# Optimization experiments

Hardware: AMD Instinct MI355X
Metric: run time of the kernel (lower is better)

## Reference

```python
import jax, jax.numpy as jnp
import numpy as np

N_QUBIT = 20
N_LAYER = 50
FEAT = 128
BATCH = 128
N_NODES = BATCH * N_QUBIT * (N_LAYER + 1)  # 130560
N_EDGES = 524288
VOCAB = N_QUBIT * (N_LAYER + 1) + 1  # 1021
NEG_SLOPE = 0.01


def setup_inputs() -> dict:
    key = jax.random.key(0)
    ks = jax.random.split(key, 32)
    s = 0.05
    x = jax.random.randint(ks[0], (N_NODES,), 0, VOCAB, dtype=jnp.int64 if jax.config.read('jax_enable_x64') else jnp.int32)
    edge_index = jax.random.randint(ks[1], (2, N_EDGES), 0, N_NODES, dtype=x.dtype)
    emb = (jax.random.normal(ks[2], (VOCAB, FEAT), jnp.float32) * s).at[0].set(0.0)  # padding_idx=0
    gcn_w = jax.random.normal(ks[3], (5, FEAT, FEAT), jnp.float32) * s
    gcn_b = jnp.zeros((5, FEAT), jnp.float32)
    mlp_dims = [(2 * FEAT, 2 * FEAT), (2 * FEAT, FEAT), (FEAT, FEAT), (FEAT, FEAT // 2), (FEAT // 2, FEAT // 2), (FEAT // 2, 1)]
    mlp = {}
    for i, (din, dout) in enumerate(mlp_dims):
        mlp[f'mw{i}'] = jax.random.normal(ks[4 + i], (din, dout), jnp.float32) * s
        mlp[f'mb{i}'] = jnp.zeros((dout,), jnp.float32)
    return dict(x=x, edge_index=edge_index, emb=emb, gcn_w=gcn_w, gcn_b=gcn_b, **mlp)


def _leaky(v):
    return jnp.where(v >= 0, v, NEG_SLOPE * v)


def _gcn(h, src, dst, W, b):
    # PyG GCNConv: h' = D^-1/2 (A+I) D^-1/2 (h W) + b, flow src -> dst
    n = h.shape[0]
    hw = h @ W
    loops = jnp.arange(n, dtype=src.dtype)
    s2 = jnp.concatenate([src, loops])
    d2 = jnp.concatenate([dst, loops])
    deg = jax.ops.segment_sum(jnp.ones(s2.shape[0], hw.dtype), d2, num_segments=n)
    dinv = jnp.where(deg > 0, jax.lax.rsqrt(deg), 0.0)
    norm = dinv[s2] * dinv[d2]  # [E+N]
    out = jax.ops.segment_sum(hw[s2] * norm[:, None], d2, num_segments=n)
    return out + b


def reference(x, edge_index, emb, gcn_w, gcn_b, mw0, mb0, mw1, mb1, mw2, mb2, mw3, mb3, mw4, mb4, mw5, mb5):
    src, dst = edge_index[0], edge_index[1]
    h = emb[x]  # [N, f]
    for i in range(4):
        h = _leaky(_gcn(h, src, dst, gcn_w[i], gcn_b[i])) + h
    h = _gcn(h, src, dst, gcn_w[4], gcn_b[4]) + h
    n, f = N_QUBIT, FEAT
    h = h.reshape(-1, n * (N_LAYER + 1), f)[:, :n, :]  # [B, n, f]
    b = h.shape[0]
    # cartesian pairs (i, j): concat(h_i, h_j) -> [B, n, n, 2f]
    xi = jnp.broadcast_to(h[:, :, None, :], (b, n, n, f))
    xj = jnp.broadcast_to(h[:, None, :, :], (b, n, n, f))
    p = jnp.concatenate([xi, xj], axis=-1)
    p = _leaky(p @ mw0 + mb0)
    p = _leaky(p @ mw1 + mb1)
    p = _leaky(p @ mw2 + mb2)
    p = _leaky(p @ mw3 + mb3)
    p = _leaky(p @ mw4 + mb4)
    p = (p @ mw5 + mb5)[..., 0]  # [B, n, n]
    p = (p + jnp.swapaxes(p, -1, -2)) / 2
    return p.reshape(-1, n * n)
```

## Files before the change

### kernel.cpp

```cpp
#include <hip/hip_runtime.h>
#include <hip/hip_bf16.h>

#define NQ 20
#define NLAY 51
#define FEAT 128
#define BATCH 128
#define NN (BATCH * NQ * NLAY)
#define NE 524288
#define NPAIR (BATCH * NQ * NQ)
#define NB (NN / 256)
#define VOCAB 1021

typedef _Float16 half8 __attribute__((ext_vector_type(8)));
typedef float floatx4 __attribute__((ext_vector_type(4)));
typedef unsigned int uint;

__device__ __forceinline__ float lrelu(float v) { return v >= 0.f ? v : 0.01f * v; }

__device__ __forceinline__ uint packhl(float v) {
    _Float16 h = (_Float16)v;
    _Float16 l = (_Float16)(v - (float)h);
    union { _Float16 f; unsigned short u; } hb, lb;
    hb.f = h; lb.f = l;
    return (uint)hb.u | ((uint)lb.u << 16);
}

__device__ __forceinline__ void unpack8(uint4 a, uint4 b, half8& hi, half8& lo) {
    union { uint u[4]; half8 h; } H, L;
    H.u[0] = __builtin_amdgcn_perm(a.y, a.x, 0x05040100u);
    H.u[1] = __builtin_amdgcn_perm(a.w, a.z, 0x05040100u);
    H.u[2] = __builtin_amdgcn_perm(b.y, b.x, 0x05040100u);
    H.u[3] = __builtin_amdgcn_perm(b.w, b.z, 0x05040100u);
    L.u[0] = __builtin_amdgcn_perm(a.y, a.x, 0x07060302u);
    L.u[1] = __builtin_amdgcn_perm(a.w, a.z, 0x07060302u);
    L.u[2] = __builtin_amdgcn_perm(b.y, b.x, 0x07060302u);
    L.u[3] = __builtin_amdgcn_perm(b.w, b.z, 0x07060302u);
    hi = H.h;
    lo = L.h;
}

__global__ void k_count(const int* __restrict__ dst, int* __restrict__ cnt) {
    int e = blockIdx.x * 256 + threadIdx.x;
    atomicAdd(&cnt[dst[e]], 1);
}

__global__ void k_offsets(const int* __restrict__ cnt, const int* __restrict__ x,
                          int* __restrict__ offs, float* __restrict__ dinv,
                          int4* __restrict__ meta, int* __restrict__ cursor,
                          int* __restrict__ flag1, int* __restrict__ idmap) {
    __shared__ int sm[256];
    __shared__ int sbase;
    int t = threadIdx.x, g = blockIdx.x * 256 + t;
    int v = cnt[g];
    sm[t] = v;
    __syncthreads();
    for (int s = 1; s < 256; s <<= 1) {
        int add = (t >= s) ? sm[t - s] : 0;
        __syncthreads();
        sm[t] += add;
        __syncthreads();
    }
    if (t == 255) sbase = atomicAdd(cursor, sm[255]);
    __syncthreads();
    int off = sbase + sm[t] - v;
    float di = rsqrtf((float)(v + 1));
    offs[g] = off;
    dinv[g] = di;
    meta[g] = make_int4(off, v, __float_as_int(di), x[g]);
    if (g % (NQ * NLAY) < NQ) flag1[g] = 1;
    if (g < 1024) idmap[g] = min(g, VOCAB - 1);
}

__global__ void k_fill(const int* __restrict__ src, const int* __restrict__ dst,
                       const int* __restrict__ offs, int* __restrict__ fill,
                       const float* __restrict__ dinv, const int* __restrict__ x,
                       int2* __restrict__ csre, int2* __restrict__ csre0,
                       int* __restrict__ flag1) {
    int e = blockIdx.x * 256 + threadIdx.x;
    int d = dst[e];
    int s = src[e];
    int pos = offs[d] + atomicAdd(&fill[d], 1);
    int wb = __float_as_int(dinv[s] * dinv[d]);
    csre[pos] = make_int2(s, wb);
    csre0[pos] = make_int2(x[s], wb);
    if (d % (NQ * NLAY) < NQ) flag1[s] = 1;
}

__global__ void k_s1pass(const int* __restrict__ flagI, const int4* __restrict__ meta,
                         const int2* __restrict__ csre, int* __restrict__ cur,
                         int4* __restrict__ recO, int* __restrict__ flagO,
                         int4* __restrict__ rec0q) {
    if (rec0q && blockIdx.x >= NB) {
        int q = (blockIdx.x - NB) * 256 + threadIdx.x;
        if (q < BATCH * NQ) {
            int b = q / NQ, i = q - b * NQ;
            int node = b * (NQ * NLAY) + i;
            int4 m = meta[node];
            float di = __int_as_float(m.z);
            int dc = min(m.y, 6);
            int2 eb[6];
#pragma unroll
            for (int j = 0; j < 6; j++) eb[j] = (j < dc) ? csre[m.x + j] : make_int2(0, 0);
            int4* r = rec0q + (size_t)q * 4;
            r[0] = make_int4(node + 1, m.y, __float_as_int(di * di), m.x);
            r[1] = make_int4(eb[0].x, eb[0].y, eb[1].x, eb[1].y);
            r[2] = make_int4(eb[2].x, eb[2].y, eb[3].x, eb[3].y);
            r[3] = make_int4(eb[4].x, eb[4].y, eb[5].x, eb[5].y);
        }
        return;
    }
    __shared__ int sm[256];
    __shared__ int sbase;
    int t = threadIdx.x, g = blockIdx.x * 256 + t;
    int v = flagI[g];
    sm[t] = v;
    __syncthreads();
    for (int s = 1; s < 256; s <<= 1) {
        int add = (t >= s) ? sm[t - s] : 0;
        __syncthreads();
        sm[t] += add;
        __syncthreads();
    }
    if (t == 255) sbase = atomicAdd(cur, sm[255]);
    __syncthreads();
    if (v) {
        int slot = sbase + sm[t] - 1;
        int4 m = meta[g];
        float di = __int_as_float(m.z);
        int dc = min(m.y, 6);
        int2 eb[6];
#pragma unroll
        for (int j = 0; j < 6; j++) eb[j] = (j < dc) ? csre[m.x + j] : make_int2(0, 0);
        int4* r = recO + (size_t)slot * 4;
        r[0] = make_int4(g + 1, m.y, __float_as_int(di * di), m.x);
        r[1] = make_int4(eb[0].x, eb[0].y, eb[1].x, eb[1].y);
        r[2] = make_int4(eb[2].x, eb[2].y, eb[3].x, eb[3].y);
        r[3] = make_int4(eb[4].x, eb[4].y, eb[5].x, eb[5].y);
        if (flagO) {
            flagO[g] = 1;
            for (int e = 0; e < m.y; e++) flagO[csre[m.x + e].x] = 1;
        }
    }
}

#define OFF_GCN 0
#define OFF_P0  81920
#define OFF_M1  147456
#define OFF_M2  180224
#define OFF_M3  196608
#define OFF_M4  204800
#define TS_TOTAL 208896

__global__ void k_tsplit_all(const float* __restrict__ gw, const float* __restrict__ mw0,
                             const float* __restrict__ mw1, const float* __restrict__ mw2,
                             const float* __restrict__ mw3, const float* __restrict__ mw4,
                             _Float16* __restrict__ hi, _Float16* __restrict__ lo) {
    int idx = blockIdx.x * 256 + threadIdx.x;
    const float* src;
    int K, N, rel;
    bool p0 = false;
    if (idx < OFF_P0) {
        int L = (idx - OFF_GCN) >> 14; rel = (idx - OFF_GCN) & 16383;
        src = gw + L * 16384; K = 128; N = 128;
    } else if (idx < OFF_M1) {
        rel = idx - OFF_P0; src = mw0; K = 128; N = 512; p0 = true;
    } else if (idx < OFF_M2) {
        rel = idx - OFF_M1;  src = mw1; K = 256; N = 128;
    } else if (idx < OFF_M3) {
        rel = idx - OFF_M2;  src = mw2; K = 128; N = 128;
    } else if (idx < OFF_M4) {
        rel = idx - OFF_M3;  src = mw3; K = 128; N = 64;
    } else {
        rel = idx - OFF_M4;  src = mw4; K = 64;  N = 64;
    }
    int kblks = K >> 5;
    int j = rel & 7;
    int lane = (rel >> 3) & 63;
    int t2 = rel >> 9;
    int kblk = t2 % kblks;
    int ntile = t2 / kblks;
    int col = ntile * 16 + (lane & 15);
    int k = kblk * 32 + ((lane >> 4) << 3) + j;
    float f;
    if (p0) {
        f = (col < 256) ? src[k * 256 + col] : src[(k + 128) * 256 + (col - 256)];
    } else {
        f = src[k * N + col];
    }
    _Float16 h = (_Float16)f;
    hi[idx] = h;
    lo[idx] = (_Float16)(f - (float)h);
}

template <int NT_N, bool LEAKY, bool BIAS, bool P0SPLIT, bool FUSEA, bool GATHA, bool LISTM>
__launch_bounds__(256, 2)
__global__ void hgemm(const float* __restrict__ A,
                      const float* __restrict__ FA, const float* __restrict__ FB,
                      const _Float16* __restrict__ Bh, const _Float16* __restrict__ Bl,
                      const float* __restrict__ bias,
                      float* __restrict__ C, float* __restrict__ C2,
                      int N, int K, const int* __restrict__ gmap,
                      const int* __restrict__ listm) {
    if (LISTM) {
        if ((unsigned)listm[blockIdx.x * 128] >= (unsigned)NN) return;
    }
    const int KB = K >> 5;
    const int lane = threadIdx.x & 63;
    const int wid = threadIdx.x >> 6;
    const int lm = lane & 15, lq = lane >> 4;
    const int m0 = blockIdx.x * 128 + wid * 32;
    const int n0t = blockIdx.y * NT_N;

    const float* arow[2];
    const float* brow[2];
#pragma unroll
    for (int mt = 0; mt < 2; mt++) {
        int row = m0 + mt * 16 + lm;
        if (FUSEA) {
            int b = row / (NQ * NQ);
            int rr = row - b * (NQ * NQ);
            int i = rr / NQ;
            int j = rr - i * NQ;
            arow[mt] = FA + (size_t)(b * NQ + i) * 256;
            brow[mt] = FB + (size_t)(b * NQ + j) * 256;
        } else if (GATHA) {
            arow[mt] = A + (size_t)gmap[row] * K;
        } else if (LISTM) {
            int lr = listm[row];
            lr = ((unsigned)lr < (unsigned)NN) ? lr : 0;
            arow[mt] = A + (size_t)lr * K;
        } else {
            arow[mt] = A + (size_t)row * K;
        }
    }

    floatx4 acc[2][NT_N];
#pragma unroll
    for (int mt = 0; mt < 2; mt++)
#pragma unroll
        for (int nt = 0; nt < NT_N; nt++) acc[mt][nt] = (floatx4)0.f;

    for (int kb = 0; kb < KB; kb++) {
        const int k0 = kb * 32 + lq * 8;
        half8 ahi[2], alo[2];
#pragma unroll
        for (int mt = 0; mt < 2; mt++) {
            floatx4 av0, av1;
            if (FUSEA) {
                floatx4 fa0 = *(const floatx4*)(arow[mt] + k0);
                floatx4 fa1 = *(const floatx4*)(arow[mt] + k0 + 4);
                floatx4 fb0 = *(const floatx4*)(brow[mt] + k0);
                floatx4 fb1 = *(const floatx4*)(brow[mt] + k0 + 4);
#pragma unroll
                for (int q = 0; q < 4; q++) {
                    av0[q] = lrelu(fa0[q] + fb0[q]);
                    av1[q] = lrelu(fa1[q] + fb1[q]);
                }
            } else {
                av0 = *(const floatx4*)(arow[mt] + k0);
                av1 = *(const floatx4*)(arow[mt] + k0 + 4);
            }
#pragma unroll
            for (int q = 0; q < 4; q++) {
                _Float16 h0 = (_Float16)av0[q];
                ahi[mt][q] = h0;
                alo[mt][q] = (_Float16)(av0[q] - (float)h0);
                _Float16 h1 = (_Float16)av1[q];
                ahi[mt][4 + q] = h1;
                alo[mt][4 + q] = (_Float16)(av1[q] - (float)h1);
            }
        }
#pragma unroll
        for (int nt = 0; nt < NT_N; nt++) {
            size_t boff = (((size_t)(n0t + nt) * KB + kb) * 64 + lane) * 8;
            half8 bhi = *(const half8*)(Bh + boff);
            half8 blo = *(const half8*)(Bl + boff);
#pragma unroll
            for (int mt = 0; mt < 2; mt++) {
                acc[mt][nt] = __builtin_amdgcn_mfma_f32_16x16x32_f16(ahi[mt], bhi, acc[mt][nt], 0, 0, 0);
                acc[mt][nt] = __builtin_amdgcn_mfma_f32_16x16x32_f16(ahi[mt], blo, acc[mt][nt], 0, 0, 0);
                acc[mt][nt] = __builtin_amdgcn_mfma_f32_16x16x32_f16(alo[mt], bhi, acc[mt][nt], 0, 0, 0);
            }
        }
    }

    int strow[2][4];
    bool svalid[2][4];
#pragma unroll
    for (int mt = 0; mt < 2; mt++)
#pragma unroll
        for (int r = 0; r < 4; r++) {
            int mlog = m0 + mt * 16 + lq * 4 + r;
            if (LISTM) {
                int sr = listm[mlog];
                svalid[mt][r] = (unsigned)sr < (unsigned)NN;
                strow[mt][r] = svalid[mt][r] ? sr : 0;
            } else {
                svalid[mt][r] = true;
                strow[mt][r] = mlog;
            }
        }

#pragma unroll
    for (int nt = 0; nt < NT_N; nt++) {
        int col = (n0t + nt) * 16 + lm;
        float bv = (BIAS || P0SPLIT) ? bias[col < 256 ? col : 0] : 0.f;
#pragma unroll
        for (int mt = 0; mt < 2; mt++) {
#pragma unroll
            for (int r = 0; r < 4; r++) {
                if (!svalid[mt][r]) continue;
                int row = strow[mt][r];
                float val = acc[mt][nt][r];
                if (P0SPLIT) {
                    if (col < 256) C[(size_t)row * 256 + col] = val + bv;
                    else C2[(size_t)row * 256 + col - 256] = val;
                } else {
                    if (BIAS) val += bv;
                    if (LEAKY) val = lrelu(val);
                    C[(size_t)row * N + col] = val;
                }
            }
        }
    }
}

template <bool LEAKY, bool FINAL>
__launch_bounds__(256, 8)
__global__ void k_lagg(const float* __restrict__ in, float* __restrict__ outp,
                       const int4* __restrict__ rec, const int2* __restrict__ csre,
                       const int* __restrict__ cntp, int fixcnt,
                       const _Float16* __restrict__ Bh, const _Float16* __restrict__ Bl,
                       const float* __restrict__ bias,
                       const _Float16* __restrict__ BhP, const _Float16* __restrict__ BlP,
                       const float* __restrict__ mb0p,
                       float* __restrict__ Abuf, float* __restrict__ Bbuf) {
    int lcnt = cntp ? *cntp : fixcnt;
    int sbase = blockIdx.x * 16;
    if (sbase >= lcnt) return;
    __shared__ uint X[16][132];
    __shared__ float R[16][132];
    __shared__ int NID[16];
    int tid = threadIdx.x;
    int sl = tid & 31;
    int grp = tid >> 5;
    const float4* in4 = (const float4*)in;
    {
        int lrow0 = grp * 2;
        int p0i = sbase + lrow0, p1i = p0i + 1;
        bool val0 = p0i < lcnt, val1 = p1i < lcnt;
        const int4* r0p = rec + (size_t)(val0 ? p0i : 0) * 4;
        const int4* r1p = rec + (size_t)(val1 ? p1i : 0) * 4;
        int4 hd0 = r0p[0], ea0 = r0p[1], eb0 = r0p[2], ec0 = r0p[3];
        int4 hd1 = r1p[0], ea1 = r1p[1], eb1 = r1p[2], ec1 = r1p[3];
        int n0 = hd0.x - 1;
        int n1 = hd1.x - 1;
        if (sl == 0) {
            NID[lrow0] = n0;
            NID[lrow0 + 1] = n1;
        }
        float s20 = __int_as_float(hd0.z), s21 = __int_as_float(hd1.z);
        float4 v0  = in4[(size_t)n0 * 32 + sl];
        float4 v1  = in4[(size_t)n1 * 32 + sl];
        float4 u00 = in4[(size_t)ea0.x * 32 + sl];
        float4 u01 = in4[(size_t)ea0.z * 32 + sl];
        float4 u02 = in4[(size_t)eb0.x * 32 + sl];
        float4 u03 = in4[(size_t)eb0.z * 32 + sl];
        float4 u04 = in4[(size_t)ec0.x * 32 + sl];
        float4 u05 = in4[(size_t)ec0.z * 32 + sl];
        float4 u10 = in4[(size_t)ea1.x * 32 + sl];
        float4 u11 = in4[(size_t)ea1.z * 32 + sl];
        float4 u12 = in4[(size_t)eb1.x * 32 + sl];
        float4 u13 = in4[(size_t)eb1.z * 32 + sl];
        float4 u14 = in4[(size_t)ec1.x * 32 + sl];
        float4 u15 = in4[(size_t)ec1.z * 32 + sl];
        *(float4*)&R[lrow0][sl * 4] = v0;
        *(float4*)&R[lrow0 + 1][sl * 4] = v1;
        float w00 = __int_as_float(ea0.y), w01 = __int_as_float(ea0.w);
        float w02 = __int_as_float(eb0.y), w03 = __int_as_float(eb0.w);
        float w04 = __int_as_float(ec0.y), w05 = __int_as_float(ec0.w);
        float w10 = __int_as_float(ea1.y), w11 = __int_as_float(ea1.w);
        float w12 = __int_as_float(eb1.y), w13 = __int_as_float(eb1.w);
        float w14 = __int_as_float(ec1.y), w15 = __int_as_float(ec1.w);
        float a0x = v0.x * s20 + u00.x * w00 + u01.x * w01 + u02.x * w02 + u03.x * w03 + u04.x * w04 + u05.x * w05;
        float a0y = v0.y * s20 + u00.y * w00 + u01.y * w01 + u02.y * w02 + u03.y * w03 + u04.y * w04 + u05.y * w05;
        float a0z = v0.z * s20 + u00.z * w00 + u01.z * w01 + u02.z * w02 + u03.z * w03 + u04.z * w04 + u05.z * w05;
        float a0w = v0.w * s20 + u00.w * w00 + u01.w * w01 + u02.w * w02 + u03.w * w03 + u04.w * w04 + u05.w * w05;
        float a1x = v1.x * s21 + u10.x * w10 + u11.x * w11 + u12.x * w12 + u13.x * w13 + u14.x * w14 + u15.x * w15;
        float a1y = v1.y * s21 + u10.y * w10 + u11.y * w11 + u12.y * w12 + u13.y * w13 + u14.y * w14 + u15.y * w15;
        float a1z = v1.z * s21 + u10.z * w10 + u11.z * w11 + u12.z * w12 + u13.z * w13 + u14.z * w14 + u15.z * w15;
        float a1w = v1.w * s21 + u10.w * w10 + u11.w * w11 + u12.w * w12 + u13.w * w13 + u14.w * w14 + u15.w * w15;
        int deg0 = val0 ? hd0.y : 0, deg1 = val1 ? hd1.y : 0;
        int dm = max(deg0, deg1);
        if (dm > 6) {
            int off0 = hd0.w, off1 = hd1.w;
            int d0c = max(deg0 - 1, 0), d1c = max(deg1 - 1, 0);
            for (int e = 6; e < dm; e += 6) {
                int2 e00 = csre[off0 + min(e,     d0c)];
                int2 e01 = csre[off0 + min(e + 1, d0c)];
                int2 e02 = csre[off0 + min(e + 2, d0c)];
                int2 e03 = csre[off0 + min(e + 3, d0c)];
                int2 e04 = csre[off0 + min(e + 4, d0c)];
                int2 e05 = csre[off0 + min(e + 5, d0c)];
                int2 e10 = csre[off1 + min(e,     d1c)];
                int2 e11 = csre[off1 + min(e + 1, d1c)];
                int2 e12 = csre[off1 + min(e + 2, d1c)];
                int2 e13 = csre[off1 + min(e + 3, d1c)];
                int2 e14 = csre[off1 + min(e + 4, d1c)];
                int2 e15 = csre[off1 + min(e + 5, d1c)];
                float4 x00 = in4[(size_t)e00.x * 32 + sl];
                float4 x01 = in4[(size_t)e01.x * 32 + sl];
                float4 x02 = in4[(size_t)e02.x * 32 + sl];
                float4 x03 = in4[(size_t)e03.x * 32 + sl];
                float4 x04 = in4[(size_t)e04.x * 32 + sl];
                float4 x05 = in4[(size_t)e05.x * 32 + sl];
                float4 x10 = in4[(size_t)e10.x * 32 + sl];
                float4 x11 = in4[(size_t)e11.x * 32 + sl];
                float4 x12 = in4[(size_t)e12.x * 32 + sl];
                float4 x13 = in4[(size_t)e13.x * 32 + sl];
                float4 x14 = in4[(size_t)e14.x * 32 + sl];
                float4 x15 = in4[(size_t)e15.x * 32 + sl];
                float q00 = (e     < deg0) ? __int_as_float(e00.y) : 0.f;
                float q01 = (e + 1 < deg0) ? __int_as_float(e01.y) : 0.f;
                float q02 = (e + 2 < deg0) ? __int_as_float(e02.y) : 0.f;
                float q03 = (e + 3 < deg0) ? __int_as_float(e03.y) : 0.f;
                float q04 = (e + 4 < deg0) ? __int_as_float(e04.y) : 0.f;
                float q05 = (e + 5 < deg0) ? __int_as_float(e05.y) : 0.f;
                float q10 = (e     < deg1) ? __int_as_float(e10.y) : 0.f;
                float q11 = (e + 1 < deg1) ? __int_as_float(e11.y) : 0.f;
                float q12 = (e + 2 < deg1) ? __int_as_float(e12.y) : 0.f;
                float q13 = (e + 3 < deg1) ? __int_as_float(e13.y) : 0.f;
                float q14 = (e + 4 < deg1) ? __int_as_float(e14.y) : 0.f;
                float q15 = (e + 5 < deg1) ? __int_as_float(e15.y) : 0.f;
                a0x += x00.x * q00 + x01.x * q01 + x02.x * q02 + x03.x * q03 + x04.x * q04 + x05.x * q05;
                a0y += x00.y * q00 + x01.y * q01 + x02.y * q02 + x03.y * q03 + x04.y * q04 + x05.y * q05;
                a0z += x00.z * q00 + x01.z * q01 + x02.z * q02 + x03.z * q03 + x04.z * q04 + x05.z * q05;
                a0w += x00.w * q00 + x01.w * q01 + x02.w * q02 + x03.w * q03 + x04.w * q04 + x05.w * q05;
                a1x += x10.x * q10 + x11.x * q11 + x12.x * q12 + x13.x * q13 + x14.x * q14 + x15.x * q15;
                a1y += x10.y * q10 + x11.y * q11 + x12.y * q12 + x13.y * q13 + x14.y * q14 + x15.y * q15;
                a1z += x10.z * q10 + x11.z * q11 + x12.z * q12 + x13.z * q13 + x14.z * q14 + x15.z * q15;
                a1w += x10.w * q10 + x11.w * q11 + x12.w * q12 + x13.w * q13 + x14.w * q14 + x15.w * q15;
            }
        }
        *(uint4*)&X[lrow0][sl * 4] =
            make_uint4(packhl(a0x), packhl(a0y), packhl(a0z), packhl(a0w));
        *(uint4*)&X[lrow0 + 1][sl * 4] =
            make_uint4(packhl(a1x), packhl(a1y), packhl(a1z), packhl(a1w));
    }
    __syncthreads();
    const int lane = tid & 63;
    const int wid = tid >> 6;
    const int lm = lane & 15, lq = lane >> 4;
    floatx4 acc[2];
    acc[0] = (floatx4)0.f;
    acc[1] = (floatx4)0.f;
#pragma unroll
    for (int kb = 0; kb < 4; kb++) {
        const int k0 = kb * 32 + lq * 8;
        uint4 pa = *(const uint4*)&X[lm][k0];
        uint4 pb = *(const uint4*)&X[lm][k0 + 4];
        half8 ahi, alo;
        unpack8(pa, pb, ahi, alo);
#pragma unroll
        for (int ntl = 0; ntl < 2; ntl++) {
            int nt = wid * 2 + ntl;
            size_t boff = (((size_t)nt * 4 + kb) * 64 + lane) * 8;
            half8 bhi = *(const half8*)(Bh + boff);
            half8 blo = *(const half8*)(Bl + boff);
            acc[ntl] = __builtin_amdgcn_mfma_f32_16x16x32_f16(ahi, bhi, acc[ntl], 0, 0, 0);
            acc[ntl] = __builtin_amdgcn_mfma_f32_16x16x32_f16(ahi, blo, acc[ntl], 0, 0, 0);
            acc[ntl] = __builtin_amdgcn_mfma_f32_16x16x32_f16(alo, bhi, acc[ntl], 0, 0, 0);
        }
    }
    if (FINAL) __syncthreads();
    int nodes[4];
    bool sval[4];
#pragma unroll
    for (int r = 0; r < 4; r++) {
        int slot = sbase + lq * 4 + r;
        sval[r] = slot < lcnt;
        nodes[r] = NID[lq * 4 + r];
    }
#pragma unroll
    for (int ntl = 0; ntl < 2; ntl++) {
        int col = (wid * 2 + ntl) * 16 + lm;
        float bv = bias[col];
#pragma unroll
        for (int r = 0; r < 4; r++) {
            if (!sval[r]) continue;
            float val = acc[ntl][r] + bv;
            if (LEAKY) val = lrelu(val);
            val += R[lq * 4 + r][col];
            if (FINAL)
                X[lq * 4 + r][col] = packhl(val);
            else
                outp[(size_t)nodes[r] * FEAT + col] = val;
        }
    }
    if (FINAL) {
        __syncthreads();
#pragma unroll
        for (int c = 0; c < 2; c++) {
            floatx4 acc4[4];
#pragma unroll
            for (int nt = 0; nt < 4; nt++) acc4[nt] = (floatx4)0.f;
#pragma unroll
            for (int kb = 0; kb < 4; kb++) {
                const int k0 = kb * 32 + lq * 8;
                uint4 pa = *(const uint4*)&X[lm][k0];
                uint4 pb = *(const uint4*)&X[lm][k0 + 4];
                half8 ahi, alo;
                unpack8(pa, pb, ahi, alo);
#pragma unroll
                for (int nt = 0; nt < 4; nt++) {
                    int T = wid * 8 + c * 4 + nt;
                    size_t boff = (((size_t)T * 4 + kb) * 64 + lane) * 8;
                    half8 bhi = *(const half8*)(BhP + boff);
                    half8 blo = *(const half8*)(BlP + boff);
                    acc4[nt] = __builtin_amdgcn_mfma_f32_16x16x32_f16(ahi, bhi, acc4[nt], 0, 0, 0);
                    acc4[nt] = __builtin_amdgcn_mfma_f32_16x16x32_f16(ahi, blo, acc4[nt], 0, 0, 0);
                    acc4[nt] = __builtin_amdgcn_mfma_f32_16x16x32_f16(alo, bhi, acc4[nt], 0, 0, 0);
                }
            }
#pragma unroll
            for (int nt = 0; nt < 4; nt++) {
                int T = wid * 8 + c * 4 + nt;
                int col = T * 16 + lm;
#pragma unroll
                for (int r = 0; r < 4; r++) {
                    int q = sbase + lq * 4 + r;
                    float val = acc4[nt][r];
                    if (col < 256) Abuf[(size_t)q * 256 + col] = val + mb0p[col];
                    else Bbuf[(size_t)q * 256 + col - 256] = val;
                }
            }
        }
    }
}

template <int KB, int NT>
__device__ __forceinline__ void pair_stage(uint (*__restrict__ X)[132],
                                           const _Float16* __restrict__ Bh,
                                           const _Float16* __restrict__ Bl,
                                           const float* __restrict__ bias,
                                           int srow, int lane) {
    const int lm = lane & 15, lq = lane >> 4;
    floatx4 acc[NT];
#pragma unroll
    for (int nt = 0; nt < NT; nt++) acc[nt] = (floatx4)0.f;
#pragma unroll
    for (int kb = 0; kb < KB; kb++) {
        const int k0 = kb * 32 + lq * 8;
        uint4 pa = *(const uint4*)&X[srow + lm][k0];
        uint4 pb = *(const uint4*)&X[srow + lm][k0 + 4];
        half8 ahi, alo;
        unpack8(pa, pb, ahi, alo);
#pragma unroll
        for (int nt = 0; nt < NT; nt++) {
            size_t boff = (((size_t)nt * KB + kb) * 64 + lane) * 8;
            half8 bhi = *(const half8*)(Bh + boff);
            half8 blo = *(const half8*)(Bl + boff);
            acc[nt] = __builtin_amdgcn_mfma_f32_16x16x32_f16(ahi, bhi, acc[nt], 0, 0, 0);
            acc[nt] = __builtin_amdgcn_mfma_f32_16x16x32_f16(ahi, blo, acc[nt], 0, 0, 0);
            acc[nt] = __builtin_amdgcn_mfma_f32_16x16x32_f16(alo, bhi, acc[nt], 0, 0, 0);
        }
    }
#pragma unroll
    for (int nt = 0; nt < NT; nt++) {
        int col = nt * 16 + lm;
        float bv = bias[col];
#pragma unroll
        for (int r = 0; r < 4; r++) {
            X[srow + lq * 4 + r][col] = packhl(lrelu(acc[nt][r] + bv));
        }
    }
}

__launch_bounds__(256, 4)
__global__ void k_pair(const float* __restrict__ FA, const float* __restrict__ FB,
                       const _Float16* __restrict__ bth, const _Float16* __restrict__ btl,
                       const float* __restrict__ mb1, const float* __restrict__ mb2,
                       const float* __restrict__ mb3, const float* __restrict__ mb4,
                       const float* __restrict__ mw5, const float* __restrict__ mb5,
                       float* __restrict__ out) {
    __shared__ uint X[64][132];
    const int lane = threadIdx.x & 63;
    const int wid = threadIdx.x >> 6;
    const int lm = lane & 15, lq = lane >> 4;
    const int srow = wid * 16;
    const int rbase = blockIdx.x * 64;

    {
        const int grow = rbase + srow + lm;
        int b = grow / (NQ * NQ);
        int rr = grow - b * (NQ * NQ);
        int i = rr / NQ;
        int j = rr - i * NQ;
        const float* arow = FA + (size_t)(b * NQ + i) * 256;
        const float* brow = FB + (size_t)(b * NQ + j) * 256;
        const _Float16* Bh = bth + OFF_M1;
        const _Float16* Bl = btl + OFF_M1;
        floatx4 acc[8];
#pragma unroll
        for (int nt = 0; nt < 8; nt++) acc[nt] = (floatx4)0.f;
        const int KB = 8;
#pragma unroll
        for (int kb = 0; kb < KB; kb++) {
            const int k0 = kb * 32 + lq * 8;
            floatx4 fa0 = *(const floatx4*)(arow + k0);
            floatx4 fa1 = *(const floatx4*)(arow + k0 + 4);
            floatx4 fb0 = *(const floatx4*)(brow + k0);
            floatx4 fb1 = *(const floatx4*)(brow + k0 + 4);
            half8 ahi, alo;
#pragma unroll
            for (int q = 0; q < 4; q++) {
                float v0 = lrelu(fa0[q] + fb0[q]);
                float v1 = lrelu(fa1[q] + fb1[q]);
                _Float16 h0 = (_Float16)v0;
                ahi[q] = h0;
                alo[q] = (_Float16)(v0 - (float)h0);
                _Float16 h1 = (_Float16)v1;
                ahi[4 + q] = h1;
                alo[4 + q] = (_Float16)(v1 - (float)h1);
            }
#pragma unroll
            for (int nt = 0; nt < 8; nt++) {
                size_t boff = (((size_t)nt * KB + kb) * 64 + lane) * 8;
                half8 bhi = *(const half8*)(Bh + boff);
                half8 blo = *(const half8*)(Bl + boff);
                acc[nt] = __builtin_amdgcn_mfma_f32_16x16x32_f16(ahi, bhi, acc[nt], 0, 0, 0);
                acc[nt] = __builtin_amdgcn_mfma_f32_16x16x32_f16(ahi, blo, acc[nt], 0, 0, 0);
                acc[nt] = __builtin_amdgcn_mfma_f32_16x16x32_f16(alo, bhi, acc[nt], 0, 0, 0);
            }
        }
#pragma unroll
        for (int nt = 0; nt < 8; nt++) {
            int col = nt * 16 + lm;
            float bv = mb1[col];
#pragma unroll
            for (int r = 0; r < 4; r++) {
                X[srow + lq * 4 + r][col] = packhl(lrelu(acc[nt][r] + bv));
            }
        }
    }
    pair_stage<4, 8>(X, bth + OFF_M2, btl + OFF_M2, mb2, srow, lane);
    pair_stage<4, 4>(X, bth + OFF_M3, btl + OFF_M3, mb3, srow, lane);
    pair_stage<2, 4>(X, bth + OFF_M4, btl + OFF_M4, mb4, srow, lane);
    {
        int row = srow + (lane >> 2);
        int part = lane & 3;
        float s = 0.f;
#pragma unroll
        for (int c4 = 0; c4 < 4; c4++) {
            int c0 = part * 16 + c4 * 4;
            uint4 u = *(const uint4*)&X[row][c0];
            const float* wp = mw5 + c0;
            uint uu[4] = {u.x, u.y, u.z, u.w};
#pragma unroll
            for (int q = 0; q < 4; q++) {
                union { unsigned short us; _Float16 f; } ch, cl;
                ch.us = (unsigned short)(uu[q] & 0xffffu);
                cl.us = (unsigned short)(uu[q] >> 16);
                s += ((float)ch.f + (float)cl.f) * wp[q];
            }
        }
        s += __shfl_xor(s, 1);
        s += __shfl_xor(s, 2);
        if (part == 0) {
            int p = rbase + row;
            int b = p / (NQ * NQ);
            int rr = p - b * (NQ * NQ);
            int i = rr / NQ, j = rr - i * NQ;
            float hv = 0.5f * (s + mb5[0]);
            atomicAdd(&out[(size_t)b * NQ * NQ + i * NQ + j], hv);
            atomicAdd(&out[(size_t)b * NQ * NQ + j * NQ + i], hv);
        }
    }
}

__global__ void k_agg0(const float* __restrict__ embW, const float* __restrict__ emb,
                       float* __restrict__ h,
                       const int4* __restrict__ meta, const int2* __restrict__ csre0,
                       const float* __restrict__ bias) {
    int tid = threadIdx.x;
    int sl = tid & 31;
    int p = blockIdx.x * 8 + (tid >> 5);
    int n0 = p * 2, n1 = n0 + 1;
    int4 m0 = meta[n0], m1 = meta[n1];
    float di0 = __int_as_float(m0.z), di1 = __int_as_float(m1.z);
    int off0 = m0.x, deg0 = m0.y;
    int off1 = m1.x, deg1 = m1.y;
    float4 v0 = ((const float4*)(embW + (size_t)m0.w * FEAT))[sl];
    float4 v1 = ((const float4*)(embW + (size_t)m1.w * FEAT))[sl];
    float4 ho0 = ((const float4*)(emb + (size_t)m0.w * FEAT))[sl];
    float4 ho1 = ((const float4*)(emb + (size_t)m1.w * FEAT))[sl];
    float s20 = di0 * di0, s21 = di1 * di1;
    float a0x = v0.x * s20, a0y = v0.y * s20, a0z = v0.z * s20, a0w = v0.w * s20;
    float a1x = v1.x * s21, a1y = v1.y * s21, a1z = v1.z * s21, a1w = v1.w * s21;
    int d0c = max(deg0 - 1, 0), d1c = max(deg1 - 1, 0);
    int dm = max(deg0, deg1);
    for (int e = 0; e < dm; e += 4) {
        int2 e00 = csre0[off0 + min(e,     d0c)];
        int2 e01 = csre0[off0 + min(e + 1, d0c)];
        int2 e02 = csre0[off0 + min(e + 2, d0c)];
        int2 e03 = csre0[off0 + min(e + 3, d0c)];
        int2 e10 = csre0[off1 + min(e,     d1c)];
        int2 e11 = csre0[off1 + min(e + 1, d1c)];
        int2 e12 = csre0[off1 + min(e + 2, d1c)];
        int2 e13 = csre0[off1 + min(e + 3, d1c)];
        float4 u00 = ((const float4*)(embW + (size_t)e00.x * FEAT))[sl];
        float4 u01 = ((const float4*)(embW + (size_t)e01.x * FEAT))[sl];
        float4 u02 = ((const float4*)(embW + (size_t)e02.x * FEAT))[sl];
        float4 u03 = ((const float4*)(embW + (size_t)e03.x * FEAT))[sl];
        float4 u10 = ((const float4*)(embW + (size_t)e10.x * FEAT))[sl];
        float4 u11 = ((const float4*)(embW + (size_t)e11.x * FEAT))[sl];
        float4 u12 = ((const float4*)(embW + (size_t)e12.x * FEAT))[sl];
        float4 u13 = ((const float4*)(embW + (size_t)e13.x * FEAT))[sl];
        float w00 = (e     < deg0) ? __int_as_float(e00.y) : 0.f;
        float w01 = (e + 1 < deg0) ? __int_as_float(e01.y) : 0.f;
        float w02 = (e + 2 < deg0) ? __int_as_float(e02.y) : 0.f;
        float w03 = (e + 3 < deg0) ? __int_as_float(e03.y) : 0.f;
        float w10 = (e     < deg1) ? __int_as_float(e10.y) : 0.f;
        float w11 = (e + 1 < deg1) ? __int_as_float(e11.y) : 0.f;
        float w12 = (e + 2 < deg1) ? __int_as_float(e12.y) : 0.f;
        float w13 = (e + 3 < deg1) ? __int_as_float(e13.y) : 0.f;
        a0x += u00.x * w00 + u01.x * w01 + u02.x * w02 + u03.x * w03;
        a0y += u00.y * w00 + u01.y * w01 + u02.y * w02 + u03.y * w03;
        a0z += u00.z * w00 + u01.z * w01 + u02.z * w02 + u03.z * w03;
        a0w += u00.w * w00 + u01.w * w01 + u02.w * w02 + u03.w * w03;
        a1x += u10.x * w10 + u11.x * w11 + u12.x * w12 + u13.x * w13;
        a1y += u10.y * w10 + u11.y * w11 + u12.y * w12 + u13.y * w13;
        a1z += u10.z * w10 + u11.z * w11 + u12.z * w12 + u13.z * w13;
        a1w += u10.w * w10 + u11.w * w11 + u12.w * w12 + u13.w * w13;
    }
    float4 bv = ((const float4*)bias)[sl];
    float4 r0, r1;
    r0.x = lrelu(a0x + bv.x) + ho0.x;
    r0.y = lrelu(a0y + bv.y) + ho0.y;
    r0.z = lrelu(a0z + bv.z) + ho0.z;
    r0.w = lrelu(a0w + bv.w) + ho0.w;
    r1.x = lrelu(a1x + bv.x) + ho1.x;
    r1.y = lrelu(a1y + bv.y) + ho1.y;
    r1.z = lrelu(a1z + bv.z) + ho1.z;
    r1.w = lrelu(a1w + bv.w) + ho1.w;
    ((float4*)(h + (size_t)n0 * FEAT))[sl] = r0;
    ((float4*)(h + (size_t)n1 * FEAT))[sl] = r1;
}

extern "C" void kernel_launch(void* const* d_in, const int* in_sizes, int n_in,
                              void* d_out, int out_size, void* d_ws, size_t ws_size,
                              hipStream_t stream) {
    const int* x = (const int*)d_in[0];
    const int* ei = (const int*)d_in[1];
    const int* e_src = ei;
    const int* e_dst = ei + NE;
    const float* emb = (const float*)d_in[2];
    const float* gw = (const float*)d_in[3];
    const float* gb = (const float*)d_in[4];
    const float* mw0 = (const float*)d_in[5];
    const float* mb0 = (const float*)d_in[6];
    const float* mw1 = (const float*)d_in[7];
    const float* mb1 = (const float*)d_in[8];
    const float* mw2 = (const float*)d_in[9];
    const float* mb2 = (const float*)d_in[10];
    const float* mw3 = (const float*)d_in[11];
    const float* mb3 = (const float*)d_in[12];
    const float* mw4 = (const float*)d_in[13];
    const float* mb4 = (const float*)d_in[14];
    const float* mw5 = (const float*)d_in[15];
    const float* mb5 = (const float*)d_in[16];
    float* out = (float*)d_out;

    float* wsf = (float*)d_ws;
    size_t o = 0;
    const size_t HSZ = (size_t)NN * FEAT;
    float* h  = wsf + o; o += HSZ;
    float* hw = wsf + o; o += HSZ;
    int* cnt   = (int*)(wsf + o); o += NN;
    int* fill  = (int*)(wsf + o); o += NN;
    int* flag1 = (int*)(wsf + o); o += NN;
    int* flag2 = (int*)(wsf + o); o += NN;
    int* flag3 = (int*)(wsf + o); o += NN;
    int* curs  = (int*)(wsf + o); o += 16;
    int* offs = (int*)(wsf + o); o += NN;
    float* dinv = wsf + o; o += NN;
    int4* meta = (int4*)(wsf + o); o += 4 * (size_t)NN;
    int2* csre  = (int2*)(wsf + o); o += 2 * (size_t)(NE + 8);
    int2* csre0 = (int2*)(wsf + o); o += 2 * (size_t)(NE + 8);
    int* idmap = (int*)(wsf + o); o += 1024;
    float* embW = wsf + o; o += (size_t)1024 * FEAT;
    float* Abuf = wsf + o; o += (size_t)BATCH * NQ * 256;
    float* Bbuf = wsf + o; o += (size_t)BATCH * NQ * 256;
    int4* rec1 = (int4*)(wsf + o); o += 16 * (size_t)NN;
    int4* rec2 = (int4*)(wsf + o); o += 16 * (size_t)NN;
    int4* rec3 = (int4*)(wsf + o); o += 16 * (size_t)NN;
    int4* rec0 = (int4*)(wsf + o); o += 16 * (size_t)(BATCH * NQ);
    _Float16* bt_hi = (_Float16*)(wsf + o); o += (TS_TOTAL + 2) / 2;
    _Float16* bt_lo = (_Float16*)(wsf + o); o += (TS_TOTAL + 2) / 2;

    hipMemsetAsync(out, 0, (size_t)NPAIR * sizeof(float), stream);

    k_tsplit_all<<<TS_TOTAL / 256, 256, 0, stream>>>(gw, mw0, mw1, mw2, mw3, mw4, bt_hi, bt_lo);

    hipMemsetAsync(cnt, 0, (5 * NN + 16) * sizeof(int), stream);
    hipMemsetAsync(csre + NE, 0, 8 * sizeof(int2), stream);
    hipMemsetAsync(csre0 + NE, 0, 8 * sizeof(int2), stream);
    k_count<<<NE / 256, 256, 0, stream>>>(e_dst, cnt);
    k_offsets<<<NB, 256, 0, stream>>>(cnt, x, offs, dinv, meta, curs + 0, flag1, idmap);
    k_fill<<<NE / 256, 256, 0, stream>>>(e_src, e_dst, offs, fill, dinv, x, csre, csre0, flag1);
    k_s1pass<<<NB + (BATCH * NQ + 255) / 256, 256, 0, stream>>>(
        flag1, meta, csre, curs + 1, rec1, flag2, rec0);
    k_s1pass<<<NB, 256, 0, stream>>>(flag2, meta, csre, curs + 2, rec2, flag3, nullptr);
    k_s1pass<<<NB, 256, 0, stream>>>(flag3, meta, csre, curs + 3, rec3, nullptr, nullptr);

    hgemm<1, false, false, false, false, true, false><<<dim3(8, 8), 256, 0, stream>>>(
        emb, nullptr, nullptr, bt_hi + OFF_GCN, bt_lo + OFF_GCN,
        nullptr, embW, nullptr, FEAT, FEAT, idmap, nullptr);
    k_agg0<<<NN / 16, 256, 0, stream>>>(embW, emb, h, meta, csre0, gb + 0 * FEAT);

    k_lagg<true, false><<<NN / 16, 256, 0, stream>>>(
        h, hw, rec3, csre, curs + 3, 0,
        bt_hi + OFF_GCN + 1 * 16384, bt_lo + OFF_GCN + 1 * 16384, gb + 1 * FEAT,
        nullptr, nullptr, nullptr, nullptr, nullptr);
    k_lagg<true, false><<<NN / 16, 256, 0, stream>>>(
        hw, h, rec2, csre, curs + 2, 0,
        bt_hi + OFF_GCN + 2 * 16384, bt_lo + OFF_GCN + 2 * 16384, gb + 2 * FEAT,
        nullptr, nullptr, nullptr, nullptr, nullptr);
    k_lagg<true, false><<<NN / 16, 256, 0, stream>>>(
        h, hw, rec1, csre, curs + 1, 0,
        bt_hi + OFF_GCN + 3 * 16384, bt_lo + OFF_GCN + 3 * 16384, gb + 3 * FEAT,
        nullptr, nullptr, nullptr, nullptr, nullptr);
    k_lagg<false, true><<<(BATCH * NQ) / 16, 256, 0, stream>>>(
        hw, nullptr, rec0, csre, nullptr, BATCH * NQ,
        bt_hi + OFF_GCN + 4 * 16384, bt_lo + OFF_GCN + 4 * 16384, gb + 4 * FEAT,
        bt_hi + OFF_P0, bt_lo + OFF_P0, mb0, Abuf, Bbuf);

    k_pair<<<NPAIR / 64, 256, 0, stream>>>(Abuf, Bbuf, bt_hi, bt_lo,
                                           mb1, mb2, mb3, mb4, mw5, mb5, out);
}
```

Baseline: 392.1 us.

## Record per-edge atomic rank in count pass and flag frontier by edge

The count kernel now stores each edge's slot from its atomicAdd, so the fill kernel can place edges without a second atomic pass and without the fill, offs and dinv arrays. Fill reads dinv and x from the packed meta record instead. Frontier propagation in the s1pass kernels moves from a per-flagged-node serial loop over its in-edges to extra blocks that scan all edges in parallel, which removes warp divergence but reads the full edge list each pass. The edge-scan blocks write the next flags in the same launch as the records, so those flags must only be read by later launches.

Result: no change. 385.4 us (-1.7%).

```diff
diff --git a/kernel.cpp b/kernel.cpp
--- a/kernel.cpp
+++ b/kernel.cpp
@@ -9,6 +9,7 @@
 #define NE 524288
 #define NPAIR (BATCH * NQ * NQ)
 #define NB (NN / 256)
+#define EB (NE / 256)
 #define VOCAB 1021
 
 typedef _Float16 half8 __attribute__((ext_vector_type(8)));
@@ -39,13 +40,13 @@
     lo = L.h;
 }
 
-__global__ void k_count(const int* __restrict__ dst, int* __restrict__ cnt) {
+__global__ void k_count(const int* __restrict__ dst, int* __restrict__ cnt,
+                        int* __restrict__ ord) {
     int e = blockIdx.x * 256 + threadIdx.x;
-    atomicAdd(&cnt[dst[e]], 1);
+    ord[e] = atomicAdd(&cnt[dst[e]], 1);
 }
 
 __global__ void k_offsets(const int* __restrict__ cnt, const int* __restrict__ x,
-                          int* __restrict__ offs, float* __restrict__ dinv,
                           int4* __restrict__ meta, int* __restrict__ cursor,
                           int* __restrict__ flag1, int* __restrict__ idmap) {
     __shared__ int sm[256];
@@ -64,48 +65,57 @@
     __syncthreads();
     int off = sbase + sm[t] - v;
     float di = rsqrtf((float)(v + 1));
-    offs[g] = off;
-    dinv[g] = di;
     meta[g] = make_int4(off, v, __float_as_int(di), x[g]);
     if (g % (NQ * NLAY) < NQ) flag1[g] = 1;
     if (g < 1024) idmap[g] = min(g, VOCAB - 1);
 }
 
 __global__ void k_fill(const int* __restrict__ src, const int* __restrict__ dst,
-                       const int* __restrict__ offs, int* __restrict__ fill,
-                       const float* __restrict__ dinv, const int* __restrict__ x,
+                       const int* __restrict__ ord, const int4* __restrict__ meta,
                        int2* __restrict__ csre, int2* __restrict__ csre0,
                        int* __restrict__ flag1) {
     int e = blockIdx.x * 256 + threadIdx.x;
     int d = dst[e];
     int s = src[e];
-    int pos = offs[d] + atomicAdd(&fill[d], 1);
-    int wb = __float_as_int(dinv[s] * dinv[d]);
+    int4 md = meta[d];
+    int4 ms = meta[s];
+    int pos = md.x + ord[e];
+    int wb = __float_as_int(__int_as_float(ms.z) * __int_as_float(md.z));
     csre[pos] = make_int2(s, wb);
-    csre0[pos] = make_int2(x[s], wb);
+    csre0[pos] = make_int2(ms.w, wb);
     if (d % (NQ * NLAY) < NQ) flag1[s] = 1;
 }
 
 __global__ void k_s1pass(const int* __restrict__ flagI, const int4* __restrict__ meta,
-                         const int2* __restrict__ csre, int* __restrict__ cur,
-                         int4* __restrict__ recO, int* __restrict__ flagO,
-                         int4* __restrict__ rec0q) {
-    if (rec0q && blockIdx.x >= NB) {
-        int q = (blockIdx.x - NB) * 256 + threadIdx.x;
-        if (q < BATCH * NQ) {
-            int b = q / NQ, i = q - b * NQ;
-            int node = b * (NQ * NLAY) + i;
-            int4 m = meta[node];
-            float di = __int_as_float(m.z);
-            int dc = min(m.y, 6);
-            int2 eb[6];
-#pragma unroll
-            for (int j = 0; j < 6; j++) eb[j] = (j < dc) ? csre[m.x + j] : make_int2(0, 0);
-            int4* r = rec0q + (size_t)q * 4;
-            r[0] = make_int4(node + 1, m.y, __float_as_int(di * di), m.x);
-            r[1] = make_int4(eb[0].x, eb[0].y, eb[1].x, eb[1].y);
-            r[2] = make_int4(eb[2].x, eb[2].y, eb[3].x, eb[3].y);
-            r[3] = make_int4(eb[4].x, eb[4].y, eb[5].x, eb[5].y);
+                         const int2* __restrict__ csre,
+                         const int* __restrict__ src, const int* __restrict__ dst,
+                         int* __restrict__ cur, int4* __restrict__ recO,
+                         int* __restrict__ flagO, int4* __restrict__ rec0q) {
+    if (blockIdx.x >= NB) {
+        int xb = blockIdx.x - NB;
+        if (flagO != nullptr && xb < EB) {
+            int e = xb * 256 + threadIdx.x;
+            if (flagI[dst[e]]) flagO[src[e]] = 1;
+            return;
+        }
+        if (rec0q != nullptr) {
+            int rb = xb - (flagO ? EB : 0);
+            int q = rb * 256 + threadIdx.x;
+            if (q < BATCH * NQ) {
+                int b = q / NQ, i = q - b * NQ;
+                int node = b * (NQ * NLAY) + i;
+                int4 m = meta[node];
+                float di = __int_as_float(m.z);
+                int dc = min(m.y, 6);
+                int2 eb[6];
+#pragma unroll
+                for (int j = 0; j < 6; j++) eb[j] = (j < dc) ? csre[m.x + j] : make_int2(0, 0);
+                int4* r = rec0q + (size_t)q * 4;
+                r[0] = make_int4(node + 1, m.y, __float_as_int(di * di), m.x);
+                r[1] = make_int4(eb[0].x, eb[0].y, eb[1].x, eb[1].y);
+                r[2] = make_int4(eb[2].x, eb[2].y, eb[3].x, eb[3].y);
+                r[3] = make_int4(eb[4].x, eb[4].y, eb[5].x, eb[5].y);
+            }
         }
         return;
     }
@@ -136,10 +146,7 @@
         r[1] = make_int4(eb[0].x, eb[0].y, eb[1].x, eb[1].y);
         r[2] = make_int4(eb[2].x, eb[2].y, eb[3].x, eb[3].y);
         r[3] = make_int4(eb[4].x, eb[4].y, eb[5].x, eb[5].y);
-        if (flagO) {
-            flagO[g] = 1;
-            for (int e = 0; e < m.y; e++) flagO[csre[m.x + e].x] = 1;
-        }
+        if (flagO) flagO[g] = 1;
     }
 }
 
@@ -777,13 +784,11 @@
     float* h  = wsf + o; o += HSZ;
     float* hw = wsf + o; o += HSZ;
     int* cnt   = (int*)(wsf + o); o += NN;
-    int* fill  = (int*)(wsf + o); o += NN;
     int* flag1 = (int*)(wsf + o); o += NN;
     int* flag2 = (int*)(wsf + o); o += NN;
     int* flag3 = (int*)(wsf + o); o += NN;
     int* curs  = (int*)(wsf + o); o += 16;
-    int* offs = (int*)(wsf + o); o += NN;
-    float* dinv = wsf + o; o += NN;
+    int* ord  = (int*)(wsf + o); o += NE;
     int4* meta = (int4*)(wsf + o); o += 4 * (size_t)NN;
     int2* csre  = (int2*)(wsf + o); o += 2 * (size_t)(NE + 8);
     int2* csre0 = (int2*)(wsf + o); o += 2 * (size_t)(NE + 8);
@@ -802,16 +807,18 @@
 
     k_tsplit_all<<<TS_TOTAL / 256, 256, 0, stream>>>(gw, mw0, mw1, mw2, mw3, mw4, bt_hi, bt_lo);
 
-    hipMemsetAsync(cnt, 0, (5 * NN + 16) * sizeof(int), stream);
+    hipMemsetAsync(cnt, 0, (4 * NN + 16) * sizeof(int), stream);
     hipMemsetAsync(csre + NE, 0, 8 * sizeof(int2), stream);
     hipMemsetAsync(csre0 + NE, 0, 8 * sizeof(int2), stream);
-    k_count<<<NE / 256, 256, 0, stream>>>(e_dst, cnt);
-    k_offsets<<<NB, 256, 0, stream>>>(cnt, x, offs, dinv, meta, curs + 0, flag1, idmap);
-    k_fill<<<NE / 256, 256, 0, stream>>>(e_src, e_dst, offs, fill, dinv, x, csre, csre0, flag1);
-    k_s1pass<<<NB + (BATCH * NQ + 255) / 256, 256, 0, stream>>>(
-        flag1, meta, csre, curs + 1, rec1, flag2, rec0);
-    k_s1pass<<<NB, 256, 0, stream>>>(flag2, meta, csre, curs + 2, rec2, flag3, nullptr);
-    k_s1pass<<<NB, 256, 0, stream>>>(flag3, meta, csre, curs + 3, rec3, nullptr, nullptr);
+    k_count<<<EB, 256, 0, stream>>>(e_dst, cnt, ord);
+    k_offsets<<<NB, 256, 0, stream>>>(cnt, x, meta, curs + 0, flag1, idmap);
+    k_fill<<<EB, 256, 0, stream>>>(e_src, e_dst, ord, meta, csre, csre0, flag1);
+    k_s1pass<<<NB + EB + (BATCH * NQ + 255) / 256, 256, 0, stream>>>(
+        flag1, meta, csre, e_src, e_dst, curs + 1, rec1, flag2, rec0);
+    k_s1pass<<<NB + EB, 256, 0, stream>>>(
+        flag2, meta, csre, e_src, e_dst, curs + 2, rec2, flag3, nullptr);
+    k_s1pass<<<NB, 256, 0, stream>>>(
+        flag3, meta, csre, e_src, e_dst, curs + 3, rec3, nullptr, nullptr);
 
     hgemm<1, false, false, false, false, true, false><<<dim3(8, 8), 256, 0, stream>>>(
         emb, nullptr, nullptr, bt_hi + OFF_GCN, bt_lo + OFF_GCN,
```
